# Kernel optimization log

Measured on AMD Instinct MI355X. Metric: run time of the kernel, lower is better.

## Reference

```python
import jax, jax.numpy as jnp
import numpy as np

DIM = 64
KSZ = 3


def _conv2d(x, w, b):
    # x: (N, C, H, W), w: (O, I, 3, 3), 'same' padding
    y = jax.lax.conv_general_dilated(
        x, w, window_strides=(1, 1), padding=[(1, 1), (1, 1)],
        dimension_numbers=("NCHW", "OIHW", "NCHW"))
    return y + b[None, :, None, None]


def setup_inputs() -> dict:
    key = jax.random.key(0)
    k1, k2, k3, k4, k5 = jax.random.split(key, 5)
    b, c, t, h, w = 2, DIM, 5, 128, 128
    x = jax.random.normal(k1, (b, c, t, h, w), dtype=jnp.float32)
    # Conv3d kernels have temporal extent 1 -> equivalent 2D kernels
    w1 = jax.random.normal(k2, (DIM, DIM, 3, 3), dtype=jnp.float32) * 0.05
    b1 = jax.random.normal(k3, (DIM,), dtype=jnp.float32) * 0.05
    w2 = jax.random.normal(k4, (KSZ * KSZ, DIM, 3, 3), dtype=jnp.float32) * 0.05
    b2 = jax.random.normal(k5, (KSZ * KSZ,), dtype=jnp.float32) * 0.05
    return {"x": x, "w1": w1, "b1": b1, "w2": w2, "b2": b2}


def reference(x, w1, b1, w2, b2):
    b, c, t, h, w = x.shape
    k = KSZ
    K = t * k * k
    # Conv3d with (1,3,3) kernel == 2D conv applied per frame
    xf = x.transpose(0, 2, 1, 3, 4).reshape(b * t, c, h, w)  # (bt, c, h, w)
    y = _conv2d(xf, w1, b1)
    y = jnp.where(y >= 0, y, 0.2 * y)  # LeakyReLU(0.2)
    ker = _conv2d(y, w2, b2)  # (bt, k*k, h, w)
    # rearrange 'b (k1 k2) t h w -> b h w (t k1 k2)'
    ker = ker.reshape(b, t, k * k, h, w).transpose(0, 3, 4, 1, 2).reshape(b, h, w, K)
    ker = ker[:, None]  # (b, 1, h, w, K)
    # kernel_normalize over last dim
    ker = ker - jnp.mean(ker, axis=-1, keepdims=True) + 1.0 / K
    # replicate pad + unfold (gather kxk neighborhoods)
    pad = (k - 1) // 2
    xp = jnp.pad(xf, ((0, 0), (0, 0), (pad, pad), (pad, pad)), mode="edge")
    patches = jnp.stack(
        [xp[:, :, i:i + h, j:j + w] for i in range(k) for j in range(k)],
        axis=-1)  # (bt, c, h, w, k*k) in (k1,k2) order like F.unfold
    # '(b t) (c k1 k2) (h w) -> b c h w (t k1 k2)'
    patches = patches.reshape(b, t, c, h, w, k * k).transpose(0, 2, 3, 4, 1, 5)
    patches = patches.reshape(b, c, h, w, K)
    return jnp.sum(patches * ker, axis=-1)  # (b, c, h, w)
```

## Files before the change

### kernel.cpp

```cpp
#include <hip/hip_runtime.h>
#include <hip/hip_bf16.h>

#define HH 128
#define WW 128
#define CC 64
#define TT 5
#define HW (HH*WW)
#define NI 10

typedef __attribute__((ext_vector_type(8))) short short8;
typedef __attribute__((ext_vector_type(4))) float f32x4;

typedef const unsigned int __attribute__((address_space(1))) gu32;
typedef unsigned int __attribute__((address_space(3))) lu32;

__device__ __forceinline__ void gl_lds16(const void* g, void* l) {
  __builtin_amdgcn_global_load_lds((gu32*)g, (lu32*)l, 16, 0, 0);
}

__device__ __forceinline__ float bf2f(unsigned int bits16) {
  union { unsigned int u; float f; } v; v.u = bits16 << 16; return v.f;
}
__device__ __forceinline__ unsigned short f2bf(float f) {
  __hip_bfloat16 h = __float2bfloat16(f);
  return *reinterpret_cast<unsigned short*>(&h);
}


__global__ __launch_bounds__(256) void pack_k(const float* __restrict__ x,
    const float* __restrict__ w1, const float* __restrict__ w2,
    unsigned short* __restrict__ xb, unsigned short* __restrict__ wb1,
    unsigned short* __restrict__ wb2) {
  __shared__ unsigned short tb[128*68];
  const int tid = threadIdx.x;
  const int bx = blockIdx.x;
  if (bx >= NI*HH) {
    int idx = (bx - NI*HH)*256 + tid;
    if (idx < 64*576) {
      int oc = idx / 576, rem = idx - oc*576, kk = rem >> 6, ic = rem & 63;
      wb1[idx] = f2bf(w1[(oc*64 + ic)*9 + kk]);
    }
    if (idx < 16*576) {
      int oc = idx / 576, rem = idx - oc*576, kk = rem >> 6, ic = rem & 63;
      wb2[idx] = (oc < 9) ? f2bf(w2[(oc*64 + ic)*9 + kk]) : (unsigned short)0;
    }
    return;
  }
  const int n = bx >> 7, h = bx & 127;
  const int bi = n / 5, ti = n - bi*5;
  const float* xp = x + ((size_t)bi*CC*TT + ti)*HW + (size_t)h*WW;
  for (int e = tid; e < 64*128; e += 256) {
    int ci = e >> 7, w = e & 127;
    tb[w*68 + ci] = f2bf(xp[(size_t)ci*TT*HW + w]);
  }
  __syncthreads();
  for (int e = tid; e < 1024; e += 256) {
    int w = e >> 3, cg = e & 7;
    uint2 lo = *(const uint2*)(&tb[w*68 + cg*8]);
    uint2 hi = *(const uint2*)(&tb[w*68 + cg*8 + 4]);
    uint4 v; v.x = lo.x; v.y = lo.y; v.z = hi.x; v.w = hi.y;
    *(uint4*)(xb + (((size_t)(n*8 + cg))*HW + (size_t)h*WW + w)*8) = v;
  }
}

__global__ __launch_bounds__(256, 2) void conv1_mfma(
    const unsigned short* __restrict__ xb, const unsigned short* __restrict__ wb1,
    const float* __restrict__ b1, unsigned short* __restrict__ yb) {
  __shared__ unsigned short xt[324*64];
  __shared__ unsigned short wt[36*512];
  const int tid = threadIdx.x;
  const int wave = tid >> 6, lane = tid & 63, q = lane >> 4, r = lane & 15;
  const int n = blockIdx.z >> 1, ocg = (blockIdx.z & 1) << 5;
  const int h0 = blockIdx.y << 4, w0 = blockIdx.x << 4;
  const int wbase = tid & ~63;

  {
    const unsigned short* wsrc = wb1 + (size_t)ocg*576;
    #pragma unroll
    for (int it = 0; it < 9; ++it) {
      int e = tid + it*256;
      int frag = e >> 6, ln = e & 63;
      int kk = frag >> 2, rem = frag & 3, half = rem >> 1, g = rem & 1;
      const unsigned short* src = wsrc + (size_t)(g*16 + (ln & 15))*576
                                  + kk*64 + half*32 + ((ln >> 4) << 3);
      gl_lds16(src, (char*)wt + ((size_t)(it*256 + wbase) << 4));
    }
  }
  const bool interior = (blockIdx.x >= 1) & (blockIdx.x <= 6) &
                        (blockIdx.y >= 1) & (blockIdx.y <= 6);
  if (interior) {
    #pragma unroll
    for (int it = 0; it < 11; ++it) {
      int e = tid + it*256;
      if (e < 2592) {
        int sp = e >> 3, c = e & 7;
        int cs = c ^ (sp & 7);
        int sr = sp / 18, sc = sp - sr*18;
        int gh = h0 + sr - 1, gw = w0 + sc - 1;
        const unsigned short* src = xb + (((size_t)(n*8 + cs))*HW + gh*WW + gw)*8;
        gl_lds16(src, (char*)xt + ((size_t)(it*256 + wbase) << 4));
      }
    }
  } else {
    for (int e = tid; e < 2592; e += 256) {
      int sp = e >> 3, c = e & 7;
      int sr = sp / 18, sc = sp - sr*18;
      int gh = h0 + sr - 1, gw = w0 + sc - 1;
      uint4 v = make_uint4(0u,0u,0u,0u);
      if (gh >= 0 && gh < HH && gw >= 0 && gw < WW)
        v = *(const uint4*)(xb + (((size_t)(n*8 + c))*HW + gh*WW + gw)*8);
      *(uint4*)(&xt[sp*64 + ((c ^ (sp & 7)) << 3)]) = v;
    }
  }
  __syncthreads();

  f32x4 zero4 = {0.f, 0.f, 0.f, 0.f};
  f32x4 acc[4][2];
  #pragma unroll
  for (int i = 0; i < 4; ++i)
    #pragma unroll
    for (int g = 0; g < 2; ++g) acc[i][g] = zero4;

  #pragma unroll
  for (int half = 0; half < 2; ++half) {
    short8 bf[6][3];
    #pragma unroll
    for (int rr = 0; rr < 6; ++rr)
      #pragma unroll
      for (int dx = 0; dx < 3; ++dx) {
        int sp = (wave*4 + rr)*18 + (r + dx);
        bf[rr][dx] = *(const short8*)(&xt[sp*64 + ((((half << 2) | q) ^ (sp & 7)) << 3)]);
      }
    #pragma unroll
    for (int kk = 0; kk < 9; ++kk) {
      const int dy = kk / 3, dx = kk - dy*3;
      short8 a0 = *(const short8*)(&wt[((kk*4 + half*2 + 0) << 9) + (lane << 3)]);
      short8 a1 = *(const short8*)(&wt[((kk*4 + half*2 + 1) << 9) + (lane << 3)]);
      #pragma unroll
      for (int i = 0; i < 4; ++i) {
        acc[i][0] = __builtin_amdgcn_mfma_f32_16x16x32_bf16(a0, bf[i+dy][dx], acc[i][0], 0, 0, 0);
        acc[i][1] = __builtin_amdgcn_mfma_f32_16x16x32_bf16(a1, bf[i+dy][dx], acc[i][1], 0, 0, 0);
      }
    }
  }

  #pragma unroll
  for (int i = 0; i < 4; ++i) {
    int py = wave*4 + i;
    unsigned short* yp = yb + ((size_t)n*HW + (h0+py)*WW + (w0+r))*64;
    #pragma unroll
    for (int g = 0; g < 2; ++g) {
      int oc0 = ocg + g*16 + (q << 2);
      f32x4 bias = *(const f32x4*)(b1 + oc0);
      float v0 = acc[i][g][0] + bias[0]; v0 = (v0 >= 0.f) ? v0 : 0.2f*v0;
      float v1 = acc[i][g][1] + bias[1]; v1 = (v1 >= 0.f) ? v1 : 0.2f*v1;
      float v2 = acc[i][g][2] + bias[2]; v2 = (v2 >= 0.f) ? v2 : 0.2f*v2;
      float v3 = acc[i][g][3] + bias[3]; v3 = (v3 >= 0.f) ? v3 : 0.2f*v3;
      uint2 pk;
      pk.x = (unsigned int)f2bf(v0) | ((unsigned int)f2bf(v1) << 16);
      pk.y = (unsigned int)f2bf(v2) | ((unsigned int)f2bf(v3) << 16);
      *(uint2*)(yp + oc0) = pk;
    }
  }
}

__global__ __launch_bounds__(256) void conv2_mfma(
    const unsigned short* __restrict__ yb, const unsigned short* __restrict__ wb2,
    const float* __restrict__ b2, float* __restrict__ ker0) {
  __shared__ unsigned short yt[180*64];
  __shared__ unsigned short wt[18*512];
  const int tid = threadIdx.x;
  const int wave = tid >> 6, lane = tid & 63, q = lane >> 4, r = lane & 15;
  const int n = blockIdx.z;
  const int h0 = blockIdx.y << 3, w0 = blockIdx.x << 4;
  const unsigned short* yn = yb + (size_t)n*HW*64;
  const int wbase = tid & ~63;

  #pragma unroll
  for (int it = 0; it < 5; ++it) {
    int e = tid + it*256;
    if (e < 1152) {
      int frag = e >> 6, ln = e & 63;
      int kk = frag >> 1, half = frag & 1;
      const unsigned short* src = wb2 + (size_t)(ln & 15)*576 + kk*64
                                  + half*32 + ((ln >> 4) << 3);
      gl_lds16(src, (char*)wt + ((size_t)(it*256 + wbase) << 4));
    }
  }
  const bool interior = (blockIdx.x >= 1) & (blockIdx.x <= 6) &
                        (blockIdx.y >= 1) & (blockIdx.y <= 14);
  if (interior) {
    #pragma unroll
    for (int it = 0; it < 6; ++it) {
      int e = tid + it*256;
      if (e < 1440) {
        int sp = e >> 3, c = e & 7;
        int cs = c ^ (sp & 7);
        int sr = sp / 18, sc = sp - sr*18;
        int gh = h0 + sr - 1, gw = w0 + sc - 1;
        const unsigned short* src = yn + ((size_t)(gh*WW + gw))*64 + (cs << 3);
        gl_lds16(src, (char*)yt + ((size_t)(it*256 + wbase) << 4));
      }
    }
  } else {
    for (int e = tid; e < 1440; e += 256) {
      int sp = e >> 3, c = e & 7;
      int sr = sp / 18, sc = sp - sr*18;
      int gh = h0 + sr - 1, gw = w0 + sc - 1;
      uint4 v = make_uint4(0u,0u,0u,0u);
      if (gh >= 0 && gh < HH && gw >= 0 && gw < WW)
        v = *(const uint4*)(yn + ((size_t)(gh*WW + gw))*64 + (c << 3));
      *(uint4*)(&yt[sp*64 + ((c ^ (sp & 7)) << 3)]) = v;
    }
  }
  __syncthreads();

  f32x4 zero4 = {0.f, 0.f, 0.f, 0.f};
  f32x4 acc[2];
  #pragma unroll
  for (int i = 0; i < 2; ++i) acc[i] = zero4;

  #pragma unroll
  for (int half = 0; half < 2; ++half) {
    short8 bf[4][3];
    #pragma unroll
    for (int rr = 0; rr < 4; ++rr)
      #pragma unroll
      for (int dx = 0; dx < 3; ++dx) {
        int sp = (wave*2 + rr)*18 + (r + dx);
        bf[rr][dx] = *(const short8*)(&yt[sp*64 + ((((half << 2) | q) ^ (sp & 7)) << 3)]);
      }
    #pragma unroll
    for (int kk = 0; kk < 9; ++kk) {
      const int dy = kk / 3, dx = kk - dy*3;
      short8 a = *(const short8*)(&wt[((kk*2 + half) << 9) + (lane << 3)]);
      #pragma unroll
      for (int i = 0; i < 2; ++i)
        acc[i] = __builtin_amdgcn_mfma_f32_16x16x32_bf16(a, bf[i+dy][dx], acc[i], 0, 0, 0);
    }
  }

  #pragma unroll
  for (int i = 0; i < 2; ++i) {
    int py = wave*2 + i;
    #pragma unroll
    for (int t2 = 0; t2 < 4; ++t2) {
      int oc = (q << 2) + t2;
      if (oc < 9)
        ker0[((size_t)n*9 + oc)*HW + (h0+py)*WW + w0 + r] = acc[i][t2] + b2[oc];
    }
  }
}

__global__ __launch_bounds__(256) void dynf_k(
    const unsigned short* __restrict__ xb, const float* __restrict__ ker0,
    float* __restrict__ out) {
  __shared__ float xs0[TT*324*4];
  __shared__ float xs1[TT*324*4];
  const int tw = threadIdx.x, th = threadIdx.y;
  const int tid = th*16 + tw;
  const int wz = blockIdx.z;
  const int bi = wz >> 2, cio = (wz & 3) << 4;
  const int h0 = blockIdx.y << 4, w0 = blockIdx.x << 4;
  const int pix = (h0+th)*WW + w0 + tw;

  float kv[45]; float s = 0.f;
  #pragma unroll
  for (int t5 = 0; t5 < TT; ++t5)
    #pragma unroll
    for (int kk = 0; kk < 9; ++kk) {
      float v = ker0[((size_t)(bi*TT + t5)*9 + kk)*HW + pix];
      kv[t5*9 + kk] = v; s += v;
    }
  const float m = (s - 1.f) * (1.f/45.f);
  #pragma unroll
  for (int qq = 0; qq < 45; ++qq) kv[qq] -= m;

  for (int co = 0; co < 2; ++co) {
    const int ci0 = cio + (co << 3);
    const int cg = ci0 >> 3;
    __syncthreads();
    for (int e = tid; e < TT*324; e += 256) {
      int t5 = e / 324, sp = e - t5*324;
      int rr = sp / 18, cc = sp - rr*18;
      int gh = min(max(h0 + rr - 1, 0), HH-1);
      int gw = min(max(w0 + cc - 1, 0), WW-1);
      uint4 raw = *(const uint4*)(xb + (((size_t)((bi*TT + t5)*8 + cg))*HW + gh*WW + gw)*8);
      xs0[(e << 2) + 0] = bf2f(raw.x & 0xffffu);
      xs0[(e << 2) + 1] = bf2f(raw.x >> 16);
      xs0[(e << 2) + 2] = bf2f(raw.y & 0xffffu);
      xs0[(e << 2) + 3] = bf2f(raw.y >> 16);
      xs1[(e << 2) + 0] = bf2f(raw.z & 0xffffu);
      xs1[(e << 2) + 1] = bf2f(raw.z >> 16);
      xs1[(e << 2) + 2] = bf2f(raw.w & 0xffffu);
      xs1[(e << 2) + 3] = bf2f(raw.w >> 16);
    }
    __syncthreads();

    #pragma unroll
    for (int p = 0; p < 2; ++p) {
      const float* plane = p ? xs1 : xs0;
      float a0 = 0.f, a1 = 0.f, a2 = 0.f, a3 = 0.f;
      #pragma unroll
      for (int t5 = 0; t5 < TT; ++t5)
        #pragma unroll
        for (int dy = 0; dy < 3; ++dy)
          #pragma unroll
          for (int dx = 0; dx < 3; ++dx) {
            f32x4 xv = *(const f32x4*)(&plane[(t5*324 + (th+dy)*18 + (tw+dx)) << 2]);
            float k = kv[t5*9 + dy*3 + dx];
            a0 = fmaf(xv[0], k, a0); a1 = fmaf(xv[1], k, a1);
            a2 = fmaf(xv[2], k, a2); a3 = fmaf(xv[3], k, a3);
          }
      float* op = out + ((size_t)(bi*CC + ci0 + p*4))*HW + pix;
      op[0] = a0; op[HW] = a1; op[2*(size_t)HW] = a2; op[3*(size_t)HW] = a3;
    }
  }
}

extern "C" void kernel_launch(void* const* d_in, const int* in_sizes, int n_in,
                              void* d_out, int out_size, void* d_ws, size_t ws_size,
                              hipStream_t stream) {
  const float* x  = (const float*)d_in[0];
  const float* w1 = (const float*)d_in[1];
  const float* b1 = (const float*)d_in[2];
  const float* w2 = (const float*)d_in[3];
  const float* b2 = (const float*)d_in[4];
  float* out = (float*)d_out;

  unsigned short* xb  = (unsigned short*)d_ws;
  unsigned short* yb  = xb + (size_t)NI*HW*64;
  float*          ker0 = (float*)(yb + (size_t)NI*HW*64);
  unsigned short* wb1 = (unsigned short*)(ker0 + (size_t)NI*9*HW);
  unsigned short* wb2 = wb1 + 64*576;

  pack_k    <<<NI*HH + 144, 256, 0, stream>>>(x, w1, w2, xb, wb1, wb2);
  conv1_mfma<<<dim3(8,8,2*NI), 256, 0, stream>>>(xb, wb1, b1, yb);
  conv2_mfma<<<dim3(8,16,NI), 256, 0, stream>>>(yb, wb2, b2, ker0);
  dynf_k    <<<dim3(8,8,8), dim3(16,16), 0, stream>>>(xb, ker0, out);
}
```

Measured before the change: 143.0 us.

## Restructure conv1 into 512-thread blocks covering all output channels over two tiles

```diff
diff --git a/kernel.cpp b/kernel.cpp
--- a/kernel.cpp
+++ b/kernel.cpp
@@ -63,104 +63,128 @@
   }
 }
 
-__global__ __launch_bounds__(256, 2) void conv1_mfma(
+#define STAGE_W1(OCBASE) do {                                               \
+    _Pragma("unroll")                                                       \
+    for (int it = 0; it < 5; ++it) {                                        \
+      int e = tid + it*512;                                                 \
+      if (e < 2304) {                                                       \
+        int frag = e >> 6, ln = e & 63;                                     \
+        int kk = frag >> 2, rem = frag & 3, half = rem >> 1, g = rem & 1;   \
+        const unsigned short* src = wb1 + (size_t)((OCBASE) + g*16 + (ln & 15))*576 \
+                                    + kk*64 + half*32 + ((ln >> 4) << 3);   \
+        gl_lds16(src, (char*)wt + ((size_t)(it*512 + wbase) << 4));         \
+      }                                                                     \
+    }                                                                       \
+  } while (0)
+
+#define STAGE_X1(W0S, INTERIOR) do {                                        \
+    if (INTERIOR) {                                                         \
+      _Pragma("unroll")                                                     \
+      for (int it = 0; it < 6; ++it) {                                      \
+        int e = tid + it*512;                                               \
+        if (e < 2592) {                                                     \
+          int sp = e >> 3, c = e & 7;                                       \
+          int cs = c ^ (sp & 7);                                            \
+          int sr = sp / 18, sc = sp - sr*18;                                \
+          int gh = h0 + sr - 1, gw = (W0S) + sc - 1;                        \
+          const unsigned short* src = xb + (((size_t)(n*8 + cs))*HW + gh*WW + gw)*8; \
+          gl_lds16(src, (char*)xt + ((size_t)(it*512 + wbase) << 4));       \
+        }                                                                   \
+      }                                                                     \
+    } else {                                                                \
+      for (int e = tid; e < 2592; e += 512) {                               \
+        int sp = e >> 3, c = e & 7;                                         \
+        int sr = sp / 18, sc = sp - sr*18;                                  \
+        int gh = h0 + sr - 1, gw = (W0S) + sc - 1;                          \
+        uint4 v = make_uint4(0u,0u,0u,0u);                                  \
+        if (gh >= 0 && gh < HH && gw >= 0 && gw < WW)                       \
+          v = *(const uint4*)(xb + (((size_t)(n*8 + c))*HW + gh*WW + gw)*8); \
+        *(uint4*)(&xt[sp*64 + ((c ^ (sp & 7)) << 3)]) = v;                  \
+      }                                                                     \
+    }                                                                       \
+  } while (0)
+
+__global__ __launch_bounds__(512, 4) void conv1_mfma(
     const unsigned short* __restrict__ xb, const unsigned short* __restrict__ wb1,
     const float* __restrict__ b1, unsigned short* __restrict__ yb) {
   __shared__ unsigned short xt[324*64];
   __shared__ unsigned short wt[36*512];
   const int tid = threadIdx.x;
   const int wave = tid >> 6, lane = tid & 63, q = lane >> 4, r = lane & 15;
-  const int n = blockIdx.z >> 1, ocg = (blockIdx.z & 1) << 5;
-  const int h0 = blockIdx.y << 4, w0 = blockIdx.x << 4;
+  const int n = blockIdx.z;
+  const int h0 = blockIdx.y << 4, w0 = blockIdx.x << 5;
   const int wbase = tid & ~63;
 
-  {
-    const unsigned short* wsrc = wb1 + (size_t)ocg*576;
-    #pragma unroll
-    for (int it = 0; it < 9; ++it) {
-      int e = tid + it*256;
-      int frag = e >> 6, ln = e & 63;
-      int kk = frag >> 2, rem = frag & 3, half = rem >> 1, g = rem & 1;
-      const unsigned short* src = wsrc + (size_t)(g*16 + (ln & 15))*576
-                                  + kk*64 + half*32 + ((ln >> 4) << 3);
-      gl_lds16(src, (char*)wt + ((size_t)(it*256 + wbase) << 4));
-    }
-  }
-  const bool interior = (blockIdx.x >= 1) & (blockIdx.x <= 6) &
-                        (blockIdx.y >= 1) & (blockIdx.y <= 6);
-  if (interior) {
-    #pragma unroll
-    for (int it = 0; it < 11; ++it) {
-      int e = tid + it*256;
-      if (e < 2592) {
-        int sp = e >> 3, c = e & 7;
-        int cs = c ^ (sp & 7);
-        int sr = sp / 18, sc = sp - sr*18;
-        int gh = h0 + sr - 1, gw = w0 + sc - 1;
-        const unsigned short* src = xb + (((size_t)(n*8 + cs))*HW + gh*WW + gw)*8;
-        gl_lds16(src, (char*)xt + ((size_t)(it*256 + wbase) << 4));
+  const bool rowInt = (blockIdx.y >= 1) & (blockIdx.y <= 6);
+  const bool int0 = rowInt & (blockIdx.x >= 1);
+  const bool int1 = rowInt & (blockIdx.x <= 2);
+
+  STAGE_W1(0);
+  STAGE_X1(w0, int0);
+  __syncthreads();
+
+  f32x4 zero4 = {0.f, 0.f, 0.f, 0.f};
+
+  #pragma unroll
+  for (int p = 0; p < 4; ++p) {
+    const int st = p >> 1, g2 = p & 1;
+    const int w0s = w0 + (st << 4);
+
+    f32x4 acc[2][2];
+    #pragma unroll
+    for (int i = 0; i < 2; ++i)
+      #pragma unroll
+      for (int g = 0; g < 2; ++g) acc[i][g] = zero4;
+
+    #pragma unroll
+    for (int half = 0; half < 2; ++half) {
+      short8 bf[4][3];
+      #pragma unroll
+      for (int rr = 0; rr < 4; ++rr)
+        #pragma unroll
+        for (int dx = 0; dx < 3; ++dx) {
+          int sp = (wave*2 + rr)*18 + (r + dx);
+          bf[rr][dx] = *(const short8*)(&xt[sp*64 + ((((half << 2) | q) ^ (sp & 7)) << 3)]);
+        }
+      #pragma unroll
+      for (int kk = 0; kk < 9; ++kk) {
+        const int dy = kk / 3, dx = kk - dy*3;
+        short8 a0 = *(const short8*)(&wt[((kk*4 + half*2 + 0) << 9) + (lane << 3)]);
+        short8 a1 = *(const short8*)(&wt[((kk*4 + half*2 + 1) << 9) + (lane << 3)]);
+        #pragma unroll
+        for (int i = 0; i < 2; ++i) {
+          acc[i][0] = __builtin_amdgcn_mfma_f32_16x16x32_bf16(a0, bf[i+dy][dx], acc[i][0], 0, 0, 0);
+          acc[i][1] = __builtin_amdgcn_mfma_f32_16x16x32_bf16(a1, bf[i+dy][dx], acc[i][1], 0, 0, 0);
+        }
       }
     }
-  } else {
-    for (int e = tid; e < 2592; e += 256) {
-      int sp = e >> 3, c = e & 7;
-      int sr = sp / 18, sc = sp - sr*18;
-      int gh = h0 + sr - 1, gw = w0 + sc - 1;
-      uint4 v = make_uint4(0u,0u,0u,0u);
-      if (gh >= 0 && gh < HH && gw >= 0 && gw < WW)
-        v = *(const uint4*)(xb + (((size_t)(n*8 + c))*HW + gh*WW + gw)*8);
-      *(uint4*)(&xt[sp*64 + ((c ^ (sp & 7)) << 3)]) = v;
-    }
-  }
-  __syncthreads();
-
-  f32x4 zero4 = {0.f, 0.f, 0.f, 0.f};
-  f32x4 acc[4][2];
-  #pragma unroll
-  for (int i = 0; i < 4; ++i)
-    #pragma unroll
-    for (int g = 0; g < 2; ++g) acc[i][g] = zero4;
-
-  #pragma unroll
-  for (int half = 0; half < 2; ++half) {
-    short8 bf[6][3];
-    #pragma unroll
-    for (int rr = 0; rr < 6; ++rr)
-      #pragma unroll
-      for (int dx = 0; dx < 3; ++dx) {
-        int sp = (wave*4 + rr)*18 + (r + dx);
-        bf[rr][dx] = *(const short8*)(&xt[sp*64 + ((((half << 2) | q) ^ (sp & 7)) << 3)]);
+
+    if (p < 3) {
+      __syncthreads();
+      STAGE_W1(((p + 1) & 1) << 5);
+      if (p == 1) STAGE_X1(w0 + 16, int1);
+    }
+
+    #pragma unroll
+    for (int i = 0; i < 2; ++i) {
+      int py = wave*2 + i;
+      unsigned short* yp = yb + ((size_t)n*HW + (h0+py)*WW + (w0s + r))*64;
+      #pragma unroll
+      for (int g = 0; g < 2; ++g) {
+        int oc0 = (g2 << 5) + g*16 + (q << 2);
+        f32x4 bias = *(const f32x4*)(b1 + oc0);
+        float v0 = acc[i][g][0] + bias[0]; v0 = (v0 >= 0.f) ? v0 : 0.2f*v0;
+        float v1 = acc[i][g][1] + bias[1]; v1 = (v1 >= 0.f) ? v1 : 0.2f*v1;
+        float v2 = acc[i][g][2] + bias[2]; v2 = (v2 >= 0.f) ? v2 : 0.2f*v2;
+        float v3 = acc[i][g][3] + bias[3]; v3 = (v3 >= 0.f) ? v3 : 0.2f*v3;
+        uint2 pk;
+        pk.x = (unsigned int)f2bf(v0) | ((unsigned int)f2bf(v1) << 16);
+        pk.y = (unsigned int)f2bf(v2) | ((unsigned int)f2bf(v3) << 16);
+        *(uint2*)(yp + oc0) = pk;
       }
-    #pragma unroll
-    for (int kk = 0; kk < 9; ++kk) {
-      const int dy = kk / 3, dx = kk - dy*3;
-      short8 a0 = *(const short8*)(&wt[((kk*4 + half*2 + 0) << 9) + (lane << 3)]);
-      short8 a1 = *(const short8*)(&wt[((kk*4 + half*2 + 1) << 9) + (lane << 3)]);
-      #pragma unroll
-      for (int i = 0; i < 4; ++i) {
-        acc[i][0] = __builtin_amdgcn_mfma_f32_16x16x32_bf16(a0, bf[i+dy][dx], acc[i][0], 0, 0, 0);
-        acc[i][1] = __builtin_amdgcn_mfma_f32_16x16x32_bf16(a1, bf[i+dy][dx], acc[i][1], 0, 0, 0);
-      }
-    }
-  }
-
-  #pragma unroll
-  for (int i = 0; i < 4; ++i) {
-    int py = wave*4 + i;
-    unsigned short* yp = yb + ((size_t)n*HW + (h0+py)*WW + (w0+r))*64;
-    #pragma unroll
-    for (int g = 0; g < 2; ++g) {
-      int oc0 = ocg + g*16 + (q << 2);
-      f32x4 bias = *(const f32x4*)(b1 + oc0);
-      float v0 = acc[i][g][0] + bias[0]; v0 = (v0 >= 0.f) ? v0 : 0.2f*v0;
-      float v1 = acc[i][g][1] + bias[1]; v1 = (v1 >= 0.f) ? v1 : 0.2f*v1;
-      float v2 = acc[i][g][2] + bias[2]; v2 = (v2 >= 0.f) ? v2 : 0.2f*v2;
-      float v3 = acc[i][g][3] + bias[3]; v3 = (v3 >= 0.f) ? v3 : 0.2f*v3;
-      uint2 pk;
-      pk.x = (unsigned int)f2bf(v0) | ((unsigned int)f2bf(v1) << 16);
-      pk.y = (unsigned int)f2bf(v2) | ((unsigned int)f2bf(v3) << 16);
-      *(uint2*)(yp + oc0) = pk;
-    }
+    }
+
+    if (p < 3) __syncthreads();
   }
 }
 
@@ -335,7 +359,7 @@
   unsigned short* wb2 = wb1 + 64*576;
 
   pack_k    <<<NI*HH + 144, 256, 0, stream>>>(x, w1, w2, xb, wb1, wb2);
-  conv1_mfma<<<dim3(8,8,2*NI), 256, 0, stream>>>(xb, wb1, b1, yb);
+  conv1_mfma<<<dim3(4,8,NI), 512, 0, stream>>>(xb, wb1, b1, yb);
   conv2_mfma<<<dim3(8,16,NI), 256, 0, stream>>>(yb, wb2, b2, ker0);
   dynf_k    <<<dim3(8,8,8), dim3(16,16), 0, stream>>>(xb, ker0, out);
 }
```

Result: no change. 143.5 us (+0.4%).
